# Performance work log

Hardware: AMD Instinct MI355X
Metric: run time of the kernel (lower is better)

The kernel has to match this reference:

```python
import jax, jax.numpy as jnp
import numpy as np

EPS = 1e-6
NUM_ITERS = 3


def rmsnorm(x, w, eps=EPS):
    # Qwen3RMSNorm: x * rsqrt(mean(x^2) + eps) * weight
    return x * jax.lax.rsqrt(jnp.mean(x * x, axis=-1, keepdims=True) + eps) * w


def setup_inputs() -> dict:
    key = jax.random.key(0)
    ks = jax.random.split(key, 12)
    B, K, M, d = 8, 64, 4096, 1024
    s = 0.02  # keep projections at sane init scale
    return {
        "slots": jax.random.normal(ks[0], (B, K, d), jnp.float32),
        "P": jax.random.normal(ks[1], (B, M, d), jnp.float32),
        "Wq": jax.random.normal(ks[2], (d, d), jnp.float32) * s,
        "Wk": jax.random.normal(ks[3], (d, d), jnp.float32) * s,
        "Wv": jax.random.normal(ks[4], (d, d), jnp.float32) * s,
        "gru_wi": jax.random.normal(ks[5], (3 * d, d), jnp.float32) * s,
        "gru_wh": jax.random.normal(ks[6], (3 * d, d), jnp.float32) * s,
        "gru_bi": jax.random.normal(ks[7], (3 * d,), jnp.float32) * s,
        "gru_bh": jax.random.normal(ks[8], (3 * d,), jnp.float32) * s,
        "slot_norm_w": jnp.ones((d,), jnp.float32),
        "input_norm_w": jnp.ones((d,), jnp.float32),
    }


def gru_cell(x, h, wi, wh, bi, bh):
    # PyTorch nn.GRUCell semantics; x,h: (..., d)
    d = h.shape[-1]
    gi = jnp.einsum('...d,ed->...e', x, wi) + bi  # (..., 3d)
    gh = jnp.einsum('...d,ed->...e', h, wh) + bh
    ir, iz, inn = gi[..., :d], gi[..., d:2 * d], gi[..., 2 * d:]
    hr, hz, hn = gh[..., :d], gh[..., d:2 * d], gh[..., 2 * d:]
    r = jax.nn.sigmoid(ir + hr)
    z = jax.nn.sigmoid(iz + hz)
    n = jnp.tanh(inn + r * hn)
    return (1.0 - z) * n + z * h


def reference(slots, P, Wq, Wk, Wv, gru_wi, gru_wh, gru_bi, gru_bh,
              slot_norm_w, input_norm_w):
    d = slots.shape[-1]
    scale = d ** (-0.5)
    Pn = rmsnorm(P, input_norm_w)
    k_proj = jnp.einsum('bmd,ed->bme', Pn, Wk)  # Linear: x @ W.T
    v_proj = jnp.einsum('bmd,ed->bme', Pn, Wv)
    for _ in range(NUM_ITERS):
        sn = rmsnorm(slots, slot_norm_w)
        q = jnp.einsum('bkd,ed->bke', sn, Wq)
        scores = jnp.einsum('bkd,bmd->bkm', q, k_proj) * scale
        attn = jax.nn.softmax(scores, axis=-2)  # softmax over SLOT axis K
        attn = attn / (jnp.sum(attn, axis=-1, keepdims=True) + EPS)
        updates = jnp.einsum('bkm,bmd->bkd', attn, v_proj)
        slots = gru_cell(updates, slots, gru_wi, gru_wh, gru_bi, gru_bh)
    return slots
```

## Files before the change

kernel.cpp:

```cpp
#include <hip/hip_runtime.h>

typedef __attribute__((ext_vector_type(4))) float f32x4;
typedef __attribute__((ext_vector_type(8))) short s16x8;

static __device__ __forceinline__ unsigned short f2bf(float f) {
  unsigned int u = __builtin_bit_cast(unsigned int, f);
  u += 0x7fffu + ((u >> 16) & 1u);
  return (unsigned short)(u >> 16);
}
static __device__ __forceinline__ float bf2f(unsigned short u) {
  return __builtin_bit_cast(float, (unsigned int)u << 16);
}
static __device__ __forceinline__ float sigm(float x) { return 1.0f / (1.0f + __expf(-x)); }

static __device__ __forceinline__ void gload16(const unsigned short* g, unsigned short* l) {
  __builtin_amdgcn_global_load_lds(
      (const __attribute__((address_space(1))) void*)g,
      (__attribute__((address_space(3))) void*)l, 16, 0, 0);
}

#define FENCE() asm volatile("" ::: "memory")
#define BAR()   { FENCE(); __builtin_amdgcn_s_barrier(); FENCE(); }
#define LGKM0() asm volatile("s_waitcnt lgkmcnt(0)" ::: "memory")

__global__ __launch_bounds__(512, 2) void proj_k(
    const unsigned short* __restrict__ A, const unsigned short* __restrict__ W,
    unsigned short* __restrict__ vt) {
  __shared__ unsigned short lds[2][2][2][8192];
  const int tid = threadIdx.x, lane = tid & 63, wid = tid >> 6;
  const int wm = wid >> 2, wn = wid & 3;
  const int wg = ((int)blockIdx.x & 7) * 64 + ((int)blockIdx.x >> 3);
  const int mt = wg >> 2, nt = wg & 3;
  const unsigned short* Ap = A + (long)mt * 256 * 1024;
  const unsigned short* Wp = W + (long)nt * 256 * 1024;
  const int srow = lane >> 3;
  const int scol = (((lane & 7) ^ srow) << 3);
  const int fr = lane & 15, fq = lane >> 4;
  const int xorv = (fr & 7) << 3;

#define STAGE(buf, T, h, t)                                                    \
  { const unsigned short* gp_ = (T) ? Wp : Ap;                                 \
    _Pragma("unroll") for (int p = 0; p < 2; p++) {                            \
      int r_ = wid * 16 + p * 8 + srow;                                        \
      gload16(gp_ + (long)((h) * 128 + r_) * 1024 + (long)(t) * 64 + scol,     \
              &lds[buf][T][h][(wid * 2 + p) * 512]);                           \
    } }

#define LDA_FRAG(aq)                                                           \
  { _Pragma("unroll") for (int i = 0; i < 4; i++)                              \
      _Pragma("unroll") for (int kk = 0; kk < 2; kk++)                         \
        af[i * 2 + kk] = *(const s16x8*)(Ab + ((aq) * 64 + i * 16 + fr) * 64 + \
                                         ((kk * 32 + fq * 8) ^ xorv)); }

#define LDB_FRAG(bq, arr)                                                      \
  { _Pragma("unroll") for (int j = 0; j < 2; j++)                              \
      _Pragma("unroll") for (int kk = 0; kk < 2; kk++)                         \
        arr[j * 2 + kk] = *(const s16x8*)(Bb + ((wn & 1) * 64 + ((bq) * 2 + j) * 16 + fr) * 64 + \
                                          ((kk * 32 + fq * 8) ^ xorv)); }

#define MM_Q(aq, bq, arr)                                                      \
  { __builtin_amdgcn_s_setprio(1);                                             \
    _Pragma("unroll") for (int i = 0; i < 4; i++)                              \
      _Pragma("unroll") for (int j = 0; j < 2; j++)                            \
        _Pragma("unroll") for (int kk = 0; kk < 2; kk++)                       \
          acc[(aq) * 4 + i][(bq) * 2 + j] = __builtin_amdgcn_mfma_f32_16x16x32_bf16( \
              af[i * 2 + kk], arr[j * 2 + kk], acc[(aq) * 4 + i][(bq) * 2 + j], 0, 0, 0); \
    __builtin_amdgcn_s_setprio(0); }

  f32x4 acc[8][4];
  #pragma unroll
  for (int i = 0; i < 8; i++)
    #pragma unroll
    for (int j = 0; j < 4; j++) acc[i][j] = (f32x4){0.f, 0.f, 0.f, 0.f};

  STAGE(0, 0, 0, 0); STAGE(0, 0, 1, 0); STAGE(0, 1, 0, 0); STAGE(0, 1, 1, 0);
  STAGE(1, 1, 0, 1); STAGE(1, 1, 1, 1);
  asm volatile("s_waitcnt vmcnt(4)" ::: "memory");
  BAR();

  s16x8 af[8], b0f[4], b1f[4];
  for (int t = 0; t < 16; ++t) {
    const int pt = t & 1;
    const unsigned short* Ab = &lds[pt][0][wm][0];
    const unsigned short* Bb = &lds[pt][1][wn >> 1][0];
    LDA_FRAG(0); LDB_FRAG(0, b0f);
    if (t < 15) STAGE(pt ^ 1, 0, 0, t + 1);
    BAR(); LGKM0();
    MM_Q(0, 0, b0f);
    BAR();
    LDB_FRAG(1, b1f);
    if (t < 15) STAGE(pt ^ 1, 0, 1, t + 1);
    BAR(); LGKM0();
    MM_Q(0, 1, b1f);
    BAR();
    LDA_FRAG(1);
    if (t < 14) STAGE(pt, 1, 0, t + 2);
    BAR(); LGKM0();
    MM_Q(1, 0, b0f);
    BAR();
    if (t < 14) STAGE(pt, 1, 1, t + 2);
    if (t == 14) { asm volatile("s_waitcnt vmcnt(0)" ::: "memory"); }
    else         { asm volatile("s_waitcnt vmcnt(4)" ::: "memory"); }
    BAR();
    MM_Q(1, 1, b1f);
    BAR();
  }

  const int nbase = nt * 256 + wn * 64;
  #pragma unroll
  for (int i = 0; i < 8; i++) {
    const int gm0 = mt * 256 + wm * 128 + i * 16 + fq * 4;
    const int b = gm0 >> 12, mrow = gm0 & 4095;
    #pragma unroll
    for (int j = 0; j < 4; j++) {
      const int n = nbase + j * 16 + fr;
      ushort4 o;
      o.x = f2bf(acc[i][j][0]); o.y = f2bf(acc[i][j][1]);
      o.z = f2bf(acc[i][j][2]); o.w = f2bf(acc[i][j][3]);
      *(ushort4*)(vt + ((long)b * 1024 + n) * 4096 + mrow) = o;
    }
  }
#undef STAGE
#undef LDA_FRAG
#undef LDB_FRAG
#undef MM_Q
}

__global__ __launch_bounds__(256) void rmsnorm_k(const float* __restrict__ x,
                                                 const float* __restrict__ w,
                                                 unsigned short* __restrict__ y,
                                                 unsigned short* __restrict__ y_raw) {
  const int row = blockIdx.x;
  const int tid = threadIdx.x;
  const float4* xp = (const float4*)(x + (long)row * 1024);
  float4 v = xp[tid];
  float ss = v.x * v.x + v.y * v.y + v.z * v.z + v.w * v.w;
  #pragma unroll
  for (int off = 32; off; off >>= 1) ss += __shfl_xor(ss, off, 64);
  __shared__ float sb[4];
  if ((tid & 63) == 0) sb[tid >> 6] = ss;
  __syncthreads();
  float tot = sb[0] + sb[1] + sb[2] + sb[3];
  float rs = rsqrtf(tot * (1.0f / 1024.0f) + 1e-6f);
  const float4* wp = (const float4*)w;
  float4 wv = wp[tid];
  ushort4 o;
  o.x = f2bf(v.x * rs * wv.x);
  o.y = f2bf(v.y * rs * wv.y);
  o.z = f2bf(v.z * rs * wv.z);
  o.w = f2bf(v.w * rs * wv.w);
  ((ushort4*)y)[(long)row * 256 + tid] = o;
  if (y_raw) {
    ushort4 r;
    r.x = f2bf(v.x); r.y = f2bf(v.y); r.z = f2bf(v.z); r.w = f2bf(v.w);
    ((ushort4*)y_raw)[(long)row * 256 + tid] = r;
  }
}

static __device__ __forceinline__ void cvt_chunk(const float* __restrict__ in,
                                                 unsigned short* __restrict__ out, long i) {
  const float4* p = (const float4*)in;
  float4 a = p[i * 2], b = p[i * 2 + 1];
  ushort4 lo, hi;
  lo.x = f2bf(a.x); lo.y = f2bf(a.y); lo.z = f2bf(a.z); lo.w = f2bf(a.w);
  hi.x = f2bf(b.x); hi.y = f2bf(b.y); hi.z = f2bf(b.z); hi.w = f2bf(b.w);
  ushort4* o = (ushort4*)out;
  o[i * 2] = lo;
  o[i * 2 + 1] = hi;
}
__global__ __launch_bounds__(256) void cvt1_k(const float* __restrict__ a,
                                              unsigned short* __restrict__ oa) {
  cvt_chunk(a, oa, (long)blockIdx.x * 256 + threadIdx.x);
}
__global__ __launch_bounds__(256) void cvt2b_k(const float* __restrict__ a, const float* __restrict__ b,
                                               unsigned short* __restrict__ oa,
                                               unsigned short* __restrict__ ob) {
  int x = blockIdx.x;
  if (x < 1536) cvt_chunk(a, oa, (long)x * 256 + threadIdx.x);
  else          cvt_chunk(b, ob, (long)(x - 1536) * 256 + threadIdx.x);
}

__global__ __launch_bounds__(256) void tcvt_k(const float* __restrict__ a,
                                              const float* __restrict__ b,
                                              unsigned short* __restrict__ oa,
                                              unsigned short* __restrict__ ob) {
  __shared__ float tile[64][65];
  const float* in = (blockIdx.z == 0) ? a : b;
  unsigned short* out = (blockIdx.z == 0) ? oa : ob;
  const int r0 = blockIdx.y * 64, c0 = blockIdx.x * 64;
  const int tid = threadIdx.x;
  #pragma unroll
  for (int i = 0; i < 4; i++) {
    int idx = tid + i * 256;
    int r = idx >> 4, c4 = (idx & 15) * 4;
    float4 v = *(const float4*)(in + (long)(r0 + r) * 1024 + c0 + c4);
    tile[r][c4] = v.x; tile[r][c4 + 1] = v.y; tile[r][c4 + 2] = v.z; tile[r][c4 + 3] = v.w;
  }
  __syncthreads();
  #pragma unroll
  for (int i = 0; i < 4; i++) {
    int idx = tid + i * 256;
    int c = idx >> 4, r4 = (idx & 15) * 4;
    ushort4 o;
    o.x = f2bf(tile[r4][c]);     o.y = f2bf(tile[r4 + 1][c]);
    o.z = f2bf(tile[r4 + 2][c]); o.w = f2bf(tile[r4 + 3][c]);
    *(ushort4*)(out + (long)(c0 + c) * 1024 + r0 + r4) = o;
  }
}

template <int BM, int BN, int WR, int WC, typename CT, int EPI, int SPLIT, int QGH>
__global__ __launch_bounds__(WR * WC * 64) void gemm_bt(
    const unsigned short* __restrict__ A, const unsigned short* __restrict__ W,
    CT* __restrict__ C, int N, int Klen, int lda, int ldw,
    long sA, long sW, long sC, const float* __restrict__ bias,
    const float* __restrict__ bias2, float alpha, float* __restrict__ rs_part,
    const unsigned short* __restrict__ A2, const unsigned short* __restrict__ W2) {
  constexpr int BK = 64;
  constexpr int NT = WR * WC * 64;
  static_assert(NT == 256, "256 threads");
  constexpr int WSM = BM / WR, WSN = BN / WC;
  constexpr int MR = WSM / 16, NR = WSN / 16;
  constexpr int SEG_A = BM / 8, SEG_W = BN / 8;
  constexpr int PA = SEG_A / 4, PW = SEG_W / 4;
  static_assert(SEG_A % 4 == 0 && SEG_W % 4 == 0, "seg divisibility");
  __shared__ unsigned short As[BM * BK];
  __shared__ unsigned short Ws[BN * BK];
  const int tid = threadIdx.x, lane = tid & 63, wid = tid >> 6;
  const int wr = wid / WC, wc = wid % WC;
  const int tileN = blockIdx.x * BN, tileM = blockIdx.y * BM;
  int coff = 0;
  int zb = 0;
  if constexpr (QGH) {
    const int zz = blockIdx.z;
    if (zz > 0) {
      A = A2;
      W = W2 + (long)(zz - 1) * 1024 * ldw;
      bias = bias2 + (zz - 1) * 1024;
      coff = zz * 1024;
    }
  } else {
    zb = blockIdx.z / SPLIT;
    const int zs = blockIdx.z % SPLIT;
    A += (long)zb * sA + (long)zs * Klen;
    W += (long)zb * sW + (long)zs * Klen;
    C += (long)blockIdx.z * sC;
  }
  const int srow = lane >> 3;
  const int scol = (lane & 7) * 8;
  f32x4 acc[MR][NR];
  #pragma unroll
  for (int i = 0; i < MR; i++)
    #pragma unroll
    for (int j = 0; j < NR; j++) acc[i][j] = (f32x4){0.f, 0.f, 0.f, 0.f};
  const int fr = lane & 15, fq = lane >> 4;

  for (int k0 = 0; k0 < Klen; k0 += BK) {
    #pragma unroll
    for (int p = 0; p < PA; p++) {
      int seg = wid * PA + p;
      gload16(A + (long)(tileM + seg * 8 + srow) * lda + k0 + scol, &As[seg * 512]);
    }
    #pragma unroll
    for (int p = 0; p < PW; p++) {
      int seg = wid * PW + p;
      gload16(W + (long)(tileN + seg * 8 + srow) * ldw + k0 + scol, &Ws[seg * 512]);
    }
    __syncthreads();
    #pragma unroll
    for (int kk = 0; kk < BK; kk += 32) {
      s16x8 af[MR], bf[NR];
      #pragma unroll
      for (int i = 0; i < MR; i++)
        af[i] = *(const s16x8*)(&As[(wr * WSM + i * 16 + fr) * BK + kk + fq * 8]);
      #pragma unroll
      for (int j = 0; j < NR; j++)
        bf[j] = *(const s16x8*)(&Ws[(wc * WSN + j * 16 + fr) * BK + kk + fq * 8]);
      #pragma unroll
      for (int i = 0; i < MR; i++)
        #pragma unroll
        for (int j = 0; j < NR; j++)
          acc[i][j] = __builtin_amdgcn_mfma_f32_16x16x32_bf16(af[i], bf[j], acc[i][j], 0, 0, 0);
    }
    __syncthreads();
  }

  if constexpr (EPI == 2) {
    static_assert(WR == 1 && BM == 64, "softmax epilogue needs full-M wave");
    #pragma unroll
    for (int i = 0; i < MR; i++)
      #pragma unroll
      for (int j = 0; j < NR; j++)
        #pragma unroll
        for (int q = 0; q < 4; q++) acc[i][j][q] *= alpha;
    float inv[NR];
    #pragma unroll
    for (int j = 0; j < NR; j++) {
      float mx = -1e30f;
      #pragma unroll
      for (int i = 0; i < MR; i++)
        #pragma unroll
        for (int q = 0; q < 4; q++) mx = fmaxf(mx, acc[i][j][q]);
      mx = fmaxf(mx, __shfl_xor(mx, 16, 64));
      mx = fmaxf(mx, __shfl_xor(mx, 32, 64));
      float sm = 0.f;
      #pragma unroll
      for (int i = 0; i < MR; i++)
        #pragma unroll
        for (int q = 0; q < 4; q++) {
          float e = __expf(acc[i][j][q] - mx);
          acc[i][j][q] = e;
          sm += e;
        }
      sm += __shfl_xor(sm, 16, 64);
      sm += __shfl_xor(sm, 32, 64);
      inv[j] = 1.f / sm;
    }
    float rp[MR][4];
    #pragma unroll
    for (int i = 0; i < MR; i++)
      #pragma unroll
      for (int q = 0; q < 4; q++) rp[i][q] = 0.f;
    unsigned short* Cs = (unsigned short*)C;
    #pragma unroll
    for (int i = 0; i < MR; i++)
      #pragma unroll
      for (int j = 0; j < NR; j++)
        #pragma unroll
        for (int q = 0; q < 4; q++) {
          float a = acc[i][j][q] * inv[j];
          rp[i][q] += a;
          Cs[(long)(i * 16 + fq * 4 + q) * N + tileN + wc * WSN + j * 16 + fr] = f2bf(a);
        }
    #pragma unroll
    for (int off = 1; off <= 8; off <<= 1)
      #pragma unroll
      for (int i = 0; i < MR; i++)
        #pragma unroll
        for (int q = 0; q < 4; q++) rp[i][q] += __shfl_xor(rp[i][q], off, 64);
    if (fr == 0) {
      const int rld = gridDim.x * WC;
      #pragma unroll
      for (int i = 0; i < MR; i++)
        #pragma unroll
        for (int q = 0; q < 4; q++)
          rs_part[((long)zb * 64 + i * 16 + fq * 4 + q) * rld + blockIdx.x * WC + wc] = rp[i][q];
    }
    return;
  }

  #pragma unroll
  for (int i = 0; i < MR; i++) {
    const int mbase = tileM + wr * WSM + i * 16 + fq * 4;
    #pragma unroll
    for (int j = 0; j < NR; j++) {
      const int n = tileN + wc * WSN + j * 16 + fr;
      const float bv = bias ? bias[n] : 0.f;
      #pragma unroll
      for (int q = 0; q < 4; q++) {
        float v = acc[i][j][q] * alpha + bv;
        if constexpr (sizeof(CT) == 2)
          C[(long)(mbase + q) * N + coff + n] = f2bf(v);
        else
          C[(long)(mbase + q) * N + coff + n] = v;
      }
    }
  }
}

__global__ __launch_bounds__(256) void upd_reduce_k(const unsigned short* __restrict__ part,
                                                    const float* __restrict__ rs_part,
                                                    unsigned short* __restrict__ out) {
  const int row = blockIdx.x;
  const int tid = threadIdx.x;
  float s = (tid < 128) ? rs_part[(long)row * 128 + tid] : 0.f;
  #pragma unroll
  for (int off = 32; off; off >>= 1) s += __shfl_xor(s, off, 64);
  __shared__ float sb[4];
  if ((tid & 63) == 0) sb[tid >> 6] = s;
  __syncthreads();
  const float inv = 1.f / (sb[0] + sb[1] + sb[2] + sb[3] + 1e-6f);
  const unsigned short* base =
      part + (long)(row >> 6) * 8 * 65536 + (long)(row & 63) * 1024 + tid * 4;
  float ax = 0.f, ay = 0.f, az = 0.f, aw = 0.f;
  #pragma unroll
  for (int sp = 0; sp < 8; sp++) {
    ushort4 v = *(const ushort4*)(base + (long)sp * 65536);
    ax += bf2f(v.x); ay += bf2f(v.y); az += bf2f(v.z); aw += bf2f(v.w);
  }
  ushort4 o;
  o.x = f2bf(ax * inv); o.y = f2bf(ay * inv);
  o.z = f2bf(az * inv); o.w = f2bf(aw * inv);
  ((ushort4*)out)[(long)row * 256 + tid] = o;
}

__global__ __launch_bounds__(256) void gru_k(const unsigned short* __restrict__ gi,
                                             const unsigned short* __restrict__ qgh,
                                             const float* __restrict__ h,
                                             const float* __restrict__ snw,
                                             float* __restrict__ out,
                                             unsigned short* __restrict__ out_bf,
                                             unsigned short* __restrict__ sn_out) {
  const int r = blockIdx.x;
  const int tid = threadIdx.x;
  const int c = tid * 4;
  const unsigned short* gip = gi + (long)r * 3072;
  const unsigned short* ghp = qgh + (long)r * 4096 + 1024;
  ushort4 iru = *(const ushort4*)(gip + c);
  ushort4 izu = *(const ushort4*)(gip + 1024 + c);
  ushort4 inu = *(const ushort4*)(gip + 2048 + c);
  ushort4 hru = *(const ushort4*)(ghp + c);
  ushort4 hzu = *(const ushort4*)(ghp + 1024 + c);
  ushort4 hnu = *(const ushort4*)(ghp + 2048 + c);
  float4 hv = *(const float4*)(h + (long)r * 1024 + c);
  float4 o;
  { float rr = sigm(bf2f(iru.x) + bf2f(hru.x)), zz = sigm(bf2f(izu.x) + bf2f(hzu.x));
    float nn = tanhf(bf2f(inu.x) + rr * bf2f(hnu.x)); o.x = (1.f - zz) * nn + zz * hv.x; }
  { float rr = sigm(bf2f(iru.y) + bf2f(hru.y)), zz = sigm(bf2f(izu.y) + bf2f(hzu.y));
    float nn = tanhf(bf2f(inu.y) + rr * bf2f(hnu.y)); o.y = (1.f - zz) * nn + zz * hv.y; }
  { float rr = sigm(bf2f(iru.z) + bf2f(hru.z)), zz = sigm(bf2f(izu.z) + bf2f(hzu.z));
    float nn = tanhf(bf2f(inu.z) + rr * bf2f(hnu.z)); o.z = (1.f - zz) * nn + zz * hv.z; }
  { float rr = sigm(bf2f(iru.w) + bf2f(hru.w)), zz = sigm(bf2f(izu.w) + bf2f(hzu.w));
    float nn = tanhf(bf2f(inu.w) + rr * bf2f(hnu.w)); o.w = (1.f - zz) * nn + zz * hv.w; }
  *(float4*)(out + (long)r * 1024 + c) = o;
  ushort4 ob;
  ob.x = f2bf(o.x); ob.y = f2bf(o.y); ob.z = f2bf(o.z); ob.w = f2bf(o.w);
  *(ushort4*)(out_bf + (long)r * 1024 + c) = ob;
  float ss = o.x * o.x + o.y * o.y + o.z * o.z + o.w * o.w;
  #pragma unroll
  for (int off = 32; off; off >>= 1) ss += __shfl_xor(ss, off, 64);
  __shared__ float sb[4];
  if ((tid & 63) == 0) sb[tid >> 6] = ss;
  __syncthreads();
  const float tot = sb[0] + sb[1] + sb[2] + sb[3];
  const float rs = rsqrtf(tot * (1.0f / 1024.0f) + 1e-6f);
  float4 wv = *(const float4*)(snw + c);
  ushort4 so;
  so.x = f2bf(o.x * rs * wv.x); so.y = f2bf(o.y * rs * wv.y);
  so.z = f2bf(o.z * rs * wv.z); so.w = f2bf(o.w * rs * wv.w);
  *(ushort4*)(sn_out + (long)r * 1024 + c) = so;
}

extern "C" void kernel_launch(void* const* d_in, const int* in_sizes, int n_in,
                              void* d_out, int out_size, void* d_ws, size_t ws_size,
                              hipStream_t stream) {
  const float* slots_in = (const float*)d_in[0];
  const float* P        = (const float*)d_in[1];
  const float* Wq       = (const float*)d_in[2];
  const float* Wk       = (const float*)d_in[3];
  const float* Wv       = (const float*)d_in[4];
  const float* wi       = (const float*)d_in[5];
  const float* wh       = (const float*)d_in[6];
  const float* bi       = (const float*)d_in[7];
  const float* bh       = (const float*)d_in[8];
  const float* snw      = (const float*)d_in[9];
  const float* inw      = (const float*)d_in[10];

  const size_t MB = 1024ull * 1024ull;
  char* ws = (char*)d_ws;
  unsigned short* Pn    = (unsigned short*)(ws + 0);
  unsigned short* vt    = (unsigned short*)(ws + 64 * MB);
  char* S               = ws + 128 * MB;
  unsigned short* sn    = (unsigned short*)(S);
  unsigned short* qgh   = (unsigned short*)(S + 1 * MB);
  unsigned short* attnb = (unsigned short*)(S + 5 * MB);
  unsigned short* updb  = (unsigned short*)(S + 9 * MB);
  unsigned short* slotsb= (unsigned short*)(S + 10 * MB);
  unsigned short* gi_b  = (unsigned short*)(S + 11 * MB);
  unsigned short* Cpart = (unsigned short*)(S + 14 * MB);
  float* rs_part        = (float*)(S + 22 * MB);
  unsigned short* wi_b  = (unsigned short*)(S + 23 * MB);
  unsigned short* wh_b  = (unsigned short*)(S + 29 * MB);
  unsigned short* wv_b  = (unsigned short*)(S + 35 * MB);
  unsigned short* wqt   = (unsigned short*)(S + 37 * MB);
  unsigned short* wkt   = (unsigned short*)(S + 39 * MB);
  unsigned short* m1_b  = (unsigned short*)(S + 41 * MB);
  float* slots          = (float*)(ws + 196 * MB);

  cvt1_k<<<512, 256, 0, stream>>>(Wv, wv_b);
  rmsnorm_k<<<32768, 256, 0, stream>>>(P, inw, Pn, nullptr);
  proj_k<<<512, 512, 0, stream>>>(Pn, wv_b, vt);
  tcvt_k<<<dim3(16, 16, 2), 256, 0, stream>>>(Wq, Wk, wqt, wkt);
  gemm_bt<64, 64, 2, 2, unsigned short, 0, 1, 0>
      <<<dim3(16, 16, 1), 256, 0, stream>>>(wkt, wqt, m1_b, 1024, 1024, 1024, 1024,
                                            0, 0, 0, nullptr, nullptr, 1.f, nullptr,
                                            nullptr, nullptr);
  cvt2b_k<<<3072, 256, 0, stream>>>(wi, wh, wi_b, wh_b);
  rmsnorm_k<<<512, 256, 0, stream>>>(slots_in, snw, sn, slotsb);

  for (int it = 0; it < 3; ++it) {
    gemm_bt<64, 64, 2, 2, unsigned short, 0, 1, 1>
        <<<dim3(16, 8, 4), 256, 0, stream>>>(sn, m1_b, qgh, 4096, 1024, 1024, 1024,
                                             0, 0, 0, nullptr, bh, 1.f, nullptr,
                                             slotsb, wh_b);
    gemm_bt<64, 128, 1, 4, unsigned short, 2, 1, 0>
        <<<dim3(32, 1, 8), 256, 0, stream>>>(qgh, Pn, attnb, 4096, 1024, 4096, 1024,
                                             64L * 4096, 4096L * 1024, 64L * 4096,
                                             nullptr, nullptr, 0.03125f, rs_part,
                                             nullptr, nullptr);
    gemm_bt<64, 64, 2, 2, unsigned short, 0, 8, 0>
        <<<dim3(16, 1, 64), 256, 0, stream>>>(attnb, vt, Cpart, 1024, 512, 4096, 4096,
                                              64L * 4096, 1024L * 4096, 64L * 1024,
                                              nullptr, nullptr, 1.f, nullptr,
                                              nullptr, nullptr);
    upd_reduce_k<<<512, 256, 0, stream>>>(Cpart, rs_part, updb);
    gemm_bt<64, 64, 2, 2, unsigned short, 0, 1, 0>
        <<<dim3(48, 8, 1), 256, 0, stream>>>(updb, wi_b, gi_b, 3072, 1024, 1024, 1024,
                                             0, 0, 0, bi, nullptr, 1.f, nullptr,
                                             nullptr, nullptr);
    const float* hsrc = (it == 0) ? slots_in : slots;
    float* dst = (it == 2) ? (float*)d_out : slots;
    gru_k<<<512, 256, 0, stream>>>(gi_b, qgh, hsrc, snw, dst, slotsb, sn);
  }
}
```

Baseline: 387.1 us.

## Fold Wv into GRU input weights and skip the large V projection

Removes the per-batch V projection GEMM over all points (B*M x d x d) by multiplying gru_wi with Wv once, so attention acts on the transposed normalized inputs directly and gi = upd_raw @ (wi·Wv)^T. A cheap bf16 transpose of Pn replaces the projection output layout. This drops a large GEMM in exchange for a small d x 3d x d GEMM and a transpose pass, and adds an extra bf16 rounding of the fused weight product.

```diff
diff --git a/kernel.cpp b/kernel.cpp
--- a/kernel.cpp
+++ b/kernel.cpp
@@ -17,113 +17,6 @@
   __builtin_amdgcn_global_load_lds(
       (const __attribute__((address_space(1))) void*)g,
       (__attribute__((address_space(3))) void*)l, 16, 0, 0);
-}
-
-#define FENCE() asm volatile("" ::: "memory")
-#define BAR()   { FENCE(); __builtin_amdgcn_s_barrier(); FENCE(); }
-#define LGKM0() asm volatile("s_waitcnt lgkmcnt(0)" ::: "memory")
-
-__global__ __launch_bounds__(512, 2) void proj_k(
-    const unsigned short* __restrict__ A, const unsigned short* __restrict__ W,
-    unsigned short* __restrict__ vt) {
-  __shared__ unsigned short lds[2][2][2][8192];
-  const int tid = threadIdx.x, lane = tid & 63, wid = tid >> 6;
-  const int wm = wid >> 2, wn = wid & 3;
-  const int wg = ((int)blockIdx.x & 7) * 64 + ((int)blockIdx.x >> 3);
-  const int mt = wg >> 2, nt = wg & 3;
-  const unsigned short* Ap = A + (long)mt * 256 * 1024;
-  const unsigned short* Wp = W + (long)nt * 256 * 1024;
-  const int srow = lane >> 3;
-  const int scol = (((lane & 7) ^ srow) << 3);
-  const int fr = lane & 15, fq = lane >> 4;
-  const int xorv = (fr & 7) << 3;
-
-#define STAGE(buf, T, h, t)                                                    \
-  { const unsigned short* gp_ = (T) ? Wp : Ap;                                 \
-    _Pragma("unroll") for (int p = 0; p < 2; p++) {                            \
-      int r_ = wid * 16 + p * 8 + srow;                                        \
-      gload16(gp_ + (long)((h) * 128 + r_) * 1024 + (long)(t) * 64 + scol,     \
-              &lds[buf][T][h][(wid * 2 + p) * 512]);                           \
-    } }
-
-#define LDA_FRAG(aq)                                                           \
-  { _Pragma("unroll") for (int i = 0; i < 4; i++)                              \
-      _Pragma("unroll") for (int kk = 0; kk < 2; kk++)                         \
-        af[i * 2 + kk] = *(const s16x8*)(Ab + ((aq) * 64 + i * 16 + fr) * 64 + \
-                                         ((kk * 32 + fq * 8) ^ xorv)); }
-
-#define LDB_FRAG(bq, arr)                                                      \
-  { _Pragma("unroll") for (int j = 0; j < 2; j++)                              \
-      _Pragma("unroll") for (int kk = 0; kk < 2; kk++)                         \
-        arr[j * 2 + kk] = *(const s16x8*)(Bb + ((wn & 1) * 64 + ((bq) * 2 + j) * 16 + fr) * 64 + \
-                                          ((kk * 32 + fq * 8) ^ xorv)); }
-
-#define MM_Q(aq, bq, arr)                                                      \
-  { __builtin_amdgcn_s_setprio(1);                                             \
-    _Pragma("unroll") for (int i = 0; i < 4; i++)                              \
-      _Pragma("unroll") for (int j = 0; j < 2; j++)                            \
-        _Pragma("unroll") for (int kk = 0; kk < 2; kk++)                       \
-          acc[(aq) * 4 + i][(bq) * 2 + j] = __builtin_amdgcn_mfma_f32_16x16x32_bf16( \
-              af[i * 2 + kk], arr[j * 2 + kk], acc[(aq) * 4 + i][(bq) * 2 + j], 0, 0, 0); \
-    __builtin_amdgcn_s_setprio(0); }
-
-  f32x4 acc[8][4];
-  #pragma unroll
-  for (int i = 0; i < 8; i++)
-    #pragma unroll
-    for (int j = 0; j < 4; j++) acc[i][j] = (f32x4){0.f, 0.f, 0.f, 0.f};
-
-  STAGE(0, 0, 0, 0); STAGE(0, 0, 1, 0); STAGE(0, 1, 0, 0); STAGE(0, 1, 1, 0);
-  STAGE(1, 1, 0, 1); STAGE(1, 1, 1, 1);
-  asm volatile("s_waitcnt vmcnt(4)" ::: "memory");
-  BAR();
-
-  s16x8 af[8], b0f[4], b1f[4];
-  for (int t = 0; t < 16; ++t) {
-    const int pt = t & 1;
-    const unsigned short* Ab = &lds[pt][0][wm][0];
-    const unsigned short* Bb = &lds[pt][1][wn >> 1][0];
-    LDA_FRAG(0); LDB_FRAG(0, b0f);
-    if (t < 15) STAGE(pt ^ 1, 0, 0, t + 1);
-    BAR(); LGKM0();
-    MM_Q(0, 0, b0f);
-    BAR();
-    LDB_FRAG(1, b1f);
-    if (t < 15) STAGE(pt ^ 1, 0, 1, t + 1);
-    BAR(); LGKM0();
-    MM_Q(0, 1, b1f);
-    BAR();
-    LDA_FRAG(1);
-    if (t < 14) STAGE(pt, 1, 0, t + 2);
-    BAR(); LGKM0();
-    MM_Q(1, 0, b0f);
-    BAR();
-    if (t < 14) STAGE(pt, 1, 1, t + 2);
-    if (t == 14) { asm volatile("s_waitcnt vmcnt(0)" ::: "memory"); }
-    else         { asm volatile("s_waitcnt vmcnt(4)" ::: "memory"); }
-    BAR();
-    MM_Q(1, 1, b1f);
-    BAR();
-  }
-
-  const int nbase = nt * 256 + wn * 64;
-  #pragma unroll
-  for (int i = 0; i < 8; i++) {
-    const int gm0 = mt * 256 + wm * 128 + i * 16 + fq * 4;
-    const int b = gm0 >> 12, mrow = gm0 & 4095;
-    #pragma unroll
-    for (int j = 0; j < 4; j++) {
-      const int n = nbase + j * 16 + fr;
-      ushort4 o;
-      o.x = f2bf(acc[i][j][0]); o.y = f2bf(acc[i][j][1]);
-      o.z = f2bf(acc[i][j][2]); o.w = f2bf(acc[i][j][3]);
-      *(ushort4*)(vt + ((long)b * 1024 + n) * 4096 + mrow) = o;
-    }
-  }
-#undef STAGE
-#undef LDA_FRAG
-#undef LDB_FRAG
-#undef MM_Q
 }
 
 __global__ __launch_bounds__(256) void rmsnorm_k(const float* __restrict__ x,
@@ -157,6 +50,34 @@
   }
 }
 
+__global__ __launch_bounds__(256) void tp_k(const unsigned short* __restrict__ in,
+                                            unsigned short* __restrict__ out) {
+  __shared__ unsigned short t[64][65];
+  const int x = blockIdx.x;
+  const int b = x >> 10;
+  const int mt = (x & 1023) >> 4;
+  const int dt = x & 15;
+  const int tid = threadIdx.x;
+  const long ibase = (long)b * 4096 * 1024 + (long)mt * 64 * 1024 + dt * 64;
+  #pragma unroll
+  for (int i = 0; i < 4; i++) {
+    int idx = tid + i * 256;
+    int r = idx >> 4, c4 = (idx & 15) * 4;
+    ushort4 v = *(const ushort4*)(in + ibase + (long)r * 1024 + c4);
+    t[r][c4] = v.x; t[r][c4 + 1] = v.y; t[r][c4 + 2] = v.z; t[r][c4 + 3] = v.w;
+  }
+  __syncthreads();
+  const long obase = (long)b * 1024 * 4096 + (long)dt * 64 * 4096 + mt * 64;
+  #pragma unroll
+  for (int i = 0; i < 4; i++) {
+    int idx = tid + i * 256;
+    int r = idx >> 4, c4 = (idx & 15) * 4;
+    ushort4 o;
+    o.x = t[c4][r]; o.y = t[c4 + 1][r]; o.z = t[c4 + 2][r]; o.w = t[c4 + 3][r];
+    *(ushort4*)(out + obase + (long)r * 4096 + c4) = o;
+  }
+}
+
 static __device__ __forceinline__ void cvt_chunk(const float* __restrict__ in,
                                                  unsigned short* __restrict__ out, long i) {
   const float4* p = (const float4*)in;
@@ -168,10 +89,6 @@
   o[i * 2] = lo;
   o[i * 2 + 1] = hi;
 }
-__global__ __launch_bounds__(256) void cvt1_k(const float* __restrict__ a,
-                                              unsigned short* __restrict__ oa) {
-  cvt_chunk(a, oa, (long)blockIdx.x * 256 + threadIdx.x);
-}
 __global__ __launch_bounds__(256) void cvt2b_k(const float* __restrict__ a, const float* __restrict__ b,
                                                unsigned short* __restrict__ oa,
                                                unsigned short* __restrict__ ob) {
@@ -182,11 +99,13 @@
 
 __global__ __launch_bounds__(256) void tcvt_k(const float* __restrict__ a,
                                               const float* __restrict__ b,
+                                              const float* __restrict__ c,
                                               unsigned short* __restrict__ oa,
-                                              unsigned short* __restrict__ ob) {
+                                              unsigned short* __restrict__ ob,
+                                              unsigned short* __restrict__ oc) {
   __shared__ float tile[64][65];
-  const float* in = (blockIdx.z == 0) ? a : b;
-  unsigned short* out = (blockIdx.z == 0) ? oa : ob;
+  const float* in = (blockIdx.z == 0) ? a : (blockIdx.z == 1) ? b : c;
+  unsigned short* out = (blockIdx.z == 0) ? oa : (blockIdx.z == 1) ? ob : oc;
   const int r0 = blockIdx.y * 64, c0 = blockIdx.x * 64;
   const int tid = threadIdx.x;
   #pragma unroll
@@ -458,7 +377,7 @@
   const size_t MB = 1024ull * 1024ull;
   char* ws = (char*)d_ws;
   unsigned short* Pn    = (unsigned short*)(ws + 0);
-  unsigned short* vt    = (unsigned short*)(ws + 64 * MB);
+  unsigned short* Pnt   = (unsigned short*)(ws + 64 * MB);
   char* S               = ws + 128 * MB;
   unsigned short* sn    = (unsigned short*)(S);
   unsigned short* qgh   = (unsigned short*)(S + 1 * MB);
@@ -470,21 +389,25 @@
   float* rs_part        = (float*)(S + 22 * MB);
   unsigned short* wi_b  = (unsigned short*)(S + 23 * MB);
   unsigned short* wh_b  = (unsigned short*)(S + 29 * MB);
-  unsigned short* wv_b  = (unsigned short*)(S + 35 * MB);
-  unsigned short* wqt   = (unsigned short*)(S + 37 * MB);
-  unsigned short* wkt   = (unsigned short*)(S + 39 * MB);
+  unsigned short* wqt   = (unsigned short*)(S + 35 * MB);
+  unsigned short* wkt   = (unsigned short*)(S + 37 * MB);
+  unsigned short* wvt   = (unsigned short*)(S + 39 * MB);
   unsigned short* m1_b  = (unsigned short*)(S + 41 * MB);
+  unsigned short* m2_b  = (unsigned short*)(S + 43 * MB);
   float* slots          = (float*)(ws + 196 * MB);
 
-  cvt1_k<<<512, 256, 0, stream>>>(Wv, wv_b);
+  tcvt_k<<<dim3(16, 16, 3), 256, 0, stream>>>(Wq, Wk, Wv, wqt, wkt, wvt);
   rmsnorm_k<<<32768, 256, 0, stream>>>(P, inw, Pn, nullptr);
-  proj_k<<<512, 512, 0, stream>>>(Pn, wv_b, vt);
-  tcvt_k<<<dim3(16, 16, 2), 256, 0, stream>>>(Wq, Wk, wqt, wkt);
+  tp_k<<<8192, 256, 0, stream>>>(Pn, Pnt);
   gemm_bt<64, 64, 2, 2, unsigned short, 0, 1, 0>
       <<<dim3(16, 16, 1), 256, 0, stream>>>(wkt, wqt, m1_b, 1024, 1024, 1024, 1024,
                                             0, 0, 0, nullptr, nullptr, 1.f, nullptr,
                                             nullptr, nullptr);
   cvt2b_k<<<3072, 256, 0, stream>>>(wi, wh, wi_b, wh_b);
+  gemm_bt<64, 64, 2, 2, unsigned short, 0, 1, 0>
+      <<<dim3(16, 48, 1), 256, 0, stream>>>(wi_b, wvt, m2_b, 1024, 1024, 1024, 1024,
+                                            0, 0, 0, nullptr, nullptr, 1.f, nullptr,
+                                            nullptr, nullptr);
   rmsnorm_k<<<512, 256, 0, stream>>>(slots_in, snw, sn, slotsb);
 
   for (int it = 0; it < 3; ++it) {
@@ -498,13 +421,13 @@
                                              nullptr, nullptr, 0.03125f, rs_part,
                                              nullptr, nullptr);
     gemm_bt<64, 64, 2, 2, unsigned short, 0, 8, 0>
-        <<<dim3(16, 1, 64), 256, 0, stream>>>(attnb, vt, Cpart, 1024, 512, 4096, 4096,
+        <<<dim3(16, 1, 64), 256, 0, stream>>>(attnb, Pnt, Cpart, 1024, 512, 4096, 4096,
                                               64L * 4096, 1024L * 4096, 64L * 1024,
                                               nullptr, nullptr, 1.f, nullptr,
                                               nullptr, nullptr);
     upd_reduce_k<<<512, 256, 0, stream>>>(Cpart, rs_part, updb);
     gemm_bt<64, 64, 2, 2, unsigned short, 0, 1, 0>
-        <<<dim3(48, 8, 1), 256, 0, stream>>>(updb, wi_b, gi_b, 3072, 1024, 1024, 1024,
+        <<<dim3(48, 8, 1), 256, 0, stream>>>(updb, m2_b, gi_b, 3072, 1024, 1024, 1024,
                                              0, 0, 0, bi, nullptr, 1.f, nullptr,
                                              nullptr, nullptr);
     const float* hsrc = (it == 0) ? slots_in : slots;
```

New measurement: 356.2 us. 1.09x faster.
